# Performance work log

Hardware: AMD Instinct MI355X
Metric: run time of the kernel (lower is better)

The kernel has to match this reference:

```python
import jax, jax.numpy as jnp
import numpy as np

N = 40000          # nodes
E = 400000         # edges (avg degree 10)
MUL0, MUL1 = 64, 32   # 64x0e + 32x1o
RAD, HID = 8, 64      # fc_neurons = [8, 64]
WNUM = 192            # tp.weight_numel = 64+64+32+32
NUM_NEIGHBORS = 10.0
INV3 = 1.0 / np.sqrt(3.0)   # wigner coeff for 1o x 1o -> 0e


def _lin(s, v, Ws, Wv, attr):
    """FullyConnectedTensorProduct(x, 1x0e attr) == per-irrep linear, fan-in normalized."""
    out_s = (s @ Ws) * attr * (1.0 / np.sqrt(Ws.shape[0]))
    out_v = jnp.einsum('nud,uv->nvd', v, Wv) * attr[..., None] * (1.0 / np.sqrt(Wv.shape[0]))
    return out_s, out_v


def setup_inputs() -> dict:
    key = jax.random.key(0)
    ks = jax.random.split(key, 16)
    return {
        'node_input':   jax.random.normal(ks[0], (N, MUL0 + 3 * MUL1), jnp.float32),
        'node_attr':    jnp.ones((N, 1), jnp.float32),
        'edge_attr':    jax.random.normal(ks[1], (E, 4), jnp.float32),   # 1x0e + 1x1o
        'edge_scalars': jax.random.uniform(ks[2], (E, RAD), jnp.float32),
        'W_sc_s': jax.random.normal(ks[3], (MUL0, MUL0), jnp.float32),
        'W_sc_v': jax.random.normal(ks[4], (MUL1, MUL1), jnp.float32),
        'W1_s':   jax.random.normal(ks[5], (MUL0, MUL0), jnp.float32),
        'W1_v':   jax.random.normal(ks[6], (MUL1, MUL1), jnp.float32),
        'W2_s':   jax.random.normal(ks[7], (MUL0 + MUL1, MUL0), jnp.float32),
        'W2_v':   jax.random.normal(ks[8], (MUL0 + MUL1, MUL1), jnp.float32),
        'W3':     jax.random.normal(ks[9], (MUL0 + MUL1, 1), jnp.float32),
        'fcW1':   jax.random.normal(ks[10], (RAD, HID), jnp.float32),
        'fcW2':   jax.random.normal(ks[11], (HID, WNUM), jnp.float32),
        'edge_src': jax.random.randint(ks[12], (E,), 0, N, jnp.int32),
        'edge_dst': jax.random.randint(ks[13], (E,), 0, N, jnp.int32),
    }


def reference(node_input, node_attr, edge_attr, edge_scalars,
              W_sc_s, W_sc_v, W1_s, W1_v, W2_s, W2_v, W3, fcW1, fcW2,
              edge_src, edge_dst):
    n = node_input.shape[0]
    s_in = node_input[:, :MUL0]                       # (N, 64)   0e
    v_in = node_input[:, MUL0:].reshape(n, MUL1, 3)   # (N, 32,3) 1o

    # self connection + first linear (FCTP with 1x0e attr)
    sc_s, sc_v = _lin(s_in, v_in, W_sc_s, W_sc_v, node_attr)
    f_s,  f_v  = _lin(s_in, v_in, W1_s,  W1_v,  node_attr)

    # radial MLP -> per-edge tensor-product weights (silu, fan-in normalized)
    h = jax.nn.silu(edge_scalars @ fcW1 * (1.0 / np.sqrt(RAD)))
    w = h @ fcW2 * (1.0 / np.sqrt(HID))               # (E, 192)
    wA, wB, wC, wD = w[:, :64], w[:, 64:128], w[:, 128:160], w[:, 160:192]

    # gather source node features
    xs = f_s[edge_src]                                # (E, 64)
    xv = f_v[edge_src]                                # (E, 32, 3)
    y0 = edge_attr[:, :1]                             # (E, 1)  0e
    y1 = edge_attr[:, 1:4]                            # (E, 3)  1o

    # 'uvu' tensor-product paths -> irreps_mid = 64x0e + 32x0e + 64x1o + 32x1o
    outA = wA * xs * y0                                            # 0e x 0e -> 0e
    outD = wD * jnp.einsum('eud,ed->eu', xv, y1) * INV3            # 1o x 1o -> 0e
    outB = wB[:, :, None] * xs[:, :, None] * y1[:, None, :]       # 0e x 1o -> 1o
    outC = wC[:, :, None] * xv * y0[:, :, None]                    # 1o x 0e -> 1o
    edge_feat = jnp.concatenate(
        [outA, outD, outB.reshape(-1, MUL0 * 3), outC.reshape(-1, MUL1 * 3)], axis=1)  # (E, 384)

    # scatter_add into destination nodes, normalized by sqrt(num_neighbors)
    agg = jax.ops.segment_sum(edge_feat, edge_dst, num_segments=n)
    agg = agg * (1.0 / np.sqrt(NUM_NEIGHBORS))

    ms = agg[:, :MUL0 + MUL1]                               # (N, 96)   0e
    mv = agg[:, MUL0 + MUL1:].reshape(n, MUL0 + MUL1, 3)    # (N, 96,3) 1o

    # lin2: mid -> output ; lin3: mid -> 0e (scalars only)
    c_s, c_v = _lin(ms, mv, W2_s, W2_v, node_attr)
    conv = jnp.concatenate([c_s, c_v.reshape(n, -1)], axis=1)
    sc   = jnp.concatenate([sc_s, sc_v.reshape(n, -1)], axis=1)
    angle = 0.1 * (ms @ W3) * node_attr * (1.0 / np.sqrt(MUL0 + MUL1))  # (N, 1)

    # sc.output_mask is all-ones here (every output irrep has a path)
    cos, sin = jnp.cos(angle), jnp.sin(angle)
    return cos * sc + sin * conv
```

## Files before the change

### kernel.cpp

```cpp
#include <hip/hip_runtime.h>
#include <math.h>

#define MUL0 64
#define MUL1 32
#define RADF 8
#define HIDF 64
#define WNUM 192
#define NODE_F 160
#define AGG_F  384
#define SWS 200

#define INV_SQRT64 0.125f
#define INV_SQRT32 0.17677669529663687f
#define INV_SQRT8  0.35355339059327373f
#define INV_SQRT96 0.10206207261596575f
#define INV_SQRT10 0.31622776601683794f
#define INV_SQRT3  0.5773502691896258f

typedef __attribute__((ext_vector_type(8))) short bf16x8;
typedef __attribute__((ext_vector_type(4))) float f32x4;

__device__ __forceinline__ float bf2f(unsigned short u) {
    return __uint_as_float((unsigned)u << 16);
}
__device__ __forceinline__ unsigned short f2bfu(float x) {
    unsigned ua = __float_as_uint(x);
    return (unsigned short)((ua + 0x7FFF + ((ua >> 16) & 1)) >> 16);
}
__device__ __forceinline__ unsigned bf16pack(float a, float b) {
    unsigned ua = __float_as_uint(a);
    unsigned ub = __float_as_uint(b);
    ua = (ua + 0x7FFF + ((ua >> 16) & 1)) >> 16;
    ub = (ub + 0x7FFF + ((ub >> 16) & 1)) >> 16;
    return ua | (ub << 16);
}
__device__ __forceinline__ int rdlane(int v, int i) {
    return __builtin_amdgcn_readlane(v, i);
}
__device__ __forceinline__ float rdlanef(float v, int i) {
    return __int_as_float(__builtin_amdgcn_readlane(__float_as_int(v), i));
}
__device__ __forceinline__ bf16x8 cvt8(float4 a, float4 b) {
    union { unsigned q[4]; bf16x8 v; } r;
    r.q[0] = bf16pack(a.x, a.y);
    r.q[1] = bf16pack(a.z, a.w);
    r.q[2] = bf16pack(b.x, b.y);
    r.q[3] = bf16pack(b.z, b.w);
    return r.v;
}

__global__ __launch_bounds__(256) void k_node_lin(
    const float* __restrict__ node_input,
    const float* __restrict__ node_attr,
    const float* __restrict__ W1_s,
    const float* __restrict__ W1_v,
    unsigned short* __restrict__ f, int N)
{
    __shared__ unsigned short s_w1s[8 * 64 * 8];
    __shared__ unsigned short s_w1v[4 * 32 * 8];
    int tid = threadIdx.x;

    for (int task = tid; task < 8 * 64; task += 256) {
        int col = task & 63, koct = task >> 6;
        const float* wp = W1_s + (size_t)(koct * 8) * MUL0 + col;
        unsigned pk0 = bf16pack(wp[0 * MUL0] * INV_SQRT64, wp[1 * MUL0] * INV_SQRT64);
        unsigned pk1 = bf16pack(wp[2 * MUL0] * INV_SQRT64, wp[3 * MUL0] * INV_SQRT64);
        unsigned pk2 = bf16pack(wp[4 * MUL0] * INV_SQRT64, wp[5 * MUL0] * INV_SQRT64);
        unsigned pk3 = bf16pack(wp[6 * MUL0] * INV_SQRT64, wp[7 * MUL0] * INV_SQRT64);
        *(uint4*)&s_w1s[task * 8] = make_uint4(pk0, pk1, pk2, pk3);
    }
    for (int task = tid; task < 4 * 32; task += 256) {
        int col = task & 31, koct = task >> 5;
        const float* wp = W1_v + (size_t)(koct * 8) * MUL1 + col;
        unsigned pk0 = bf16pack(wp[0 * MUL1] * INV_SQRT32, wp[1 * MUL1] * INV_SQRT32);
        unsigned pk1 = bf16pack(wp[2 * MUL1] * INV_SQRT32, wp[3 * MUL1] * INV_SQRT32);
        unsigned pk2 = bf16pack(wp[4 * MUL1] * INV_SQRT32, wp[5 * MUL1] * INV_SQRT32);
        unsigned pk3 = bf16pack(wp[6 * MUL1] * INV_SQRT32, wp[7 * MUL1] * INV_SQRT32);
        *(uint4*)&s_w1v[task * 8] = make_uint4(pk0, pk1, pk2, pk3);
    }
    __syncthreads();

    int lane = tid & 63;
    int wv = tid >> 6;
    int l15 = lane & 15, lh = lane >> 4;
    int ntiles = (N + 15) >> 4;

    for (int tile = blockIdx.x * 4 + wv; tile < ntiles; tile += gridDim.x * 4) {
        int n0 = tile << 4;
        int m = min(16, N - n0);
        int nrow = n0 + min(l15, m - 1);
        const float* inn = node_input + (size_t)nrow * NODE_F;

        float attr[4];
        #pragma unroll
        for (int r = 0; r < 4; ++r)
            attr[r] = node_attr[n0 + min(lh * 4 + r, m - 1)];

        bf16x8 inS[2];
        #pragma unroll
        for (int kk = 0; kk < 2; ++kk) {
            const float* p0 = inn + kk * 32 + lh * 8;
            inS[kk] = cvt8(*(const float4*)p0, *(const float4*)(p0 + 4));
        }
        #pragma unroll
        for (int cb = 0; cb < 4; ++cb) {
            f32x4 a = {0.f, 0.f, 0.f, 0.f};
            #pragma unroll
            for (int kk = 0; kk < 2; ++kk) {
                bf16x8 b = *(const bf16x8*)&s_w1s[(((kk * 4 + lh) * 64) + cb * 16 + l15) * 8];
                a = __builtin_amdgcn_mfma_f32_16x16x32_bf16(inS[kk], b, a, 0, 0, 0);
            }
            #pragma unroll
            for (int r = 0; r < 4; ++r) {
                int node = lh * 4 + r;
                if (node < m)
                    f[(size_t)(n0 + node) * NODE_F + cb * 16 + l15] = f2bfu(a[r] * attr[r]);
            }
        }

        #pragma unroll
        for (int d = 0; d < 3; ++d) {
            float t[8];
            #pragma unroll
            for (int j = 0; j < 8; ++j)
                t[j] = inn[64 + (lh * 8 + j) * 3 + d];
            bf16x8 inV = cvt8(make_float4(t[0], t[1], t[2], t[3]),
                              make_float4(t[4], t[5], t[6], t[7]));
            #pragma unroll
            for (int cb = 0; cb < 2; ++cb) {
                bf16x8 b = *(const bf16x8*)&s_w1v[((lh * 32) + cb * 16 + l15) * 8];
                f32x4 a = {0.f, 0.f, 0.f, 0.f};
                a = __builtin_amdgcn_mfma_f32_16x16x32_bf16(inV, b, a, 0, 0, 0);
                #pragma unroll
                for (int r = 0; r < 4; ++r) {
                    int node = lh * 4 + r;
                    if (node < m)
                        f[(size_t)(n0 + node) * NODE_F + 64 + d * 32 + cb * 16 + l15] =
                            f2bfu(a[r] * attr[r]);
                }
            }
        }
    }
}

__global__ void k_count(const int* __restrict__ edge_dst, int* deg, int E)
{
    int e = blockIdx.x * blockDim.x + threadIdx.x;
    if (e < E) atomicAdd(&deg[edge_dst[e]], 1);
}

__global__ __launch_bounds__(1024) void k_scan_a(const int* __restrict__ deg,
                                                 int* __restrict__ off,
                                                 int* __restrict__ bsum, int N)
{
    __shared__ int swsum[16];
    __shared__ int swoff[16];
    __shared__ int stot;
    int lane = threadIdx.x & 63, wid = threadIdx.x >> 6;
    int ng4 = (N + 3) >> 2;
    int g = blockIdx.x * 1024 + threadIdx.x;
    int4 v = make_int4(0, 0, 0, 0);
    if (g < ng4) v = ((const int4*)deg)[g];
    int s = v.x + v.y + v.z + v.w;
    int val = s;
    #pragma unroll
    for (int sh = 1; sh < 64; sh <<= 1) {
        int t = __shfl_up(val, sh);
        if (lane >= sh) val += t;
    }
    if (lane == 63) swsum[wid] = val;
    __syncthreads();
    if (threadIdx.x < 16) {
        int x = swsum[threadIdx.x];
        int xv = x;
        #pragma unroll
        for (int sh = 1; sh < 16; sh <<= 1) {
            int t = __shfl_up(xv, sh);
            if ((int)threadIdx.x >= sh) xv += t;
        }
        swoff[threadIdx.x] = xv - x;
        if (threadIdx.x == 15) stot = xv;
    }
    __syncthreads();
    if (g < ng4) {
        int b0 = swoff[wid] + (val - s);
        int4 o;
        o.x = b0; o.y = b0 + v.x; o.z = o.y + v.y; o.w = o.z + v.z;
        ((int4*)off)[g] = o;
    }
    if (threadIdx.x == 0) bsum[blockIdx.x] = stot;
}

__global__ __launch_bounds__(1024) void k_scan_b(int* __restrict__ off,
                                                 int* __restrict__ cur,
                                                 const int* __restrict__ bsum,
                                                 int N, int nb)
{
    __shared__ int sbase;
    if (threadIdx.x == 0) {
        int s = 0;
        for (int j = 0; j < (int)blockIdx.x; ++j) s += bsum[j];
        sbase = s;
    }
    __syncthreads();
    int base = sbase;
    int ng4 = (N + 3) >> 2;
    int g = blockIdx.x * 1024 + threadIdx.x;
    if (g < ng4) {
        int4 o = ((int4*)off)[g];
        o.x += base; o.y += base; o.z += base; o.w += base;
        ((int4*)off)[g] = o;
        ((int4*)cur)[g] = o;
    }
}

__global__ void k_scatter(const int* __restrict__ edge_dst,
                          int* cur, int* __restrict__ csr, int E)
{
    int e = blockIdx.x * blockDim.x + threadIdx.x;
    if (e < E) {
        int d = edge_dst[e];
        int pos = atomicAdd(&cur[d], 1);
        csr[pos] = e;
    }
}

#define FLUSH_AGG(node, AT)                                          \
    do {                                                             \
        float* an = agg + (size_t)(node) * AGG_F;                    \
        if (AT) {                                                    \
            atomicAdd(&an[lane], accA);                              \
            atomicAdd(&an[96  + lane], accB0);                       \
            atomicAdd(&an[192 + lane], accB1);                       \
            atomicAdd(&an[288 + lane], accB2);                       \
            if (lane < 32) {                                         \
                atomicAdd(&an[160 + u], accX0);                      \
                atomicAdd(&an[256 + u], accX1);                      \
                atomicAdd(&an[352 + u], accX2);                      \
            } else {                                                 \
                atomicAdd(&an[64 + u], accX0);                       \
            }                                                        \
        } else {                                                     \
            an[lane] = accA;                                         \
            an[96  + lane] = accB0;                                  \
            an[192 + lane] = accB1;                                  \
            an[288 + lane] = accB2;                                  \
            if (lane < 32) {                                         \
                an[160 + u] = accX0;                                 \
                an[256 + u] = accX1;                                 \
                an[352 + u] = accX2;                                 \
            } else {                                                 \
                an[64 + u] = accX0;                                  \
            }                                                        \
        }                                                            \
    } while (0)

__global__ __launch_bounds__(512, 2) void k_edge_fused(
    const unsigned short* __restrict__ f,
    const float* __restrict__ edge_scalars,
    const float* __restrict__ edge_attr,
    const float* __restrict__ fcW1,
    const float* __restrict__ fcW2,
    const int* __restrict__ edge_src,
    const int* __restrict__ edge_dst,
    const int* __restrict__ csr,
    const int* __restrict__ off,
    float* agg, int E)
{
    __shared__ unsigned short s_w2t[8 * 192 * 8];
    __shared__ unsigned short s_w[8][16 * SWS];
    __shared__ float s_fcW1[512];
    __shared__ float4 s_ea8[8][16];

    int tid  = threadIdx.x;
    int lane = tid & 63;
    int wv   = tid >> 6;
    int l15  = lane & 15, lh = lane >> 4;
    int u    = lane & 31;

    for (int task = tid; task < 1536; task += 512) {
        int col = task % 192, oct = task / 192;
        const float* wp = fcW2 + (size_t)(oct * 8) * WNUM + col;
        unsigned pk0 = bf16pack(wp[0 * WNUM], wp[1 * WNUM]);
        unsigned pk1 = bf16pack(wp[2 * WNUM], wp[3 * WNUM]);
        unsigned pk2 = bf16pack(wp[4 * WNUM], wp[5 * WNUM]);
        unsigned pk3 = bf16pack(wp[6 * WNUM], wp[7 * WNUM]);
        *(uint4*)&s_w2t[oct * 1536 + col * 8] = make_uint4(pk0, pk1, pk2, pk3);
    }
    for (int i = tid; i < 512; i += 512)
        s_fcW1[i] = fcW1[i];
    __syncthreads();

    unsigned short* sw = s_w[wv];
    float4* sea = s_ea8[wv];
    int nwt = (E + 15) >> 4;
    int stride8 = gridDim.x * 8;

    int wt = blockIdx.x * 8 + wv;
    if (wt >= nwt) return;

    int P = wt << 4;
    int m = min(16, E - P);
    int e0 = csr[P + min(l15, m - 1)];
    int src = edge_src[e0];
    int dst = edge_dst[e0];
    float4 ea = *(const float4*)(edge_attr + (size_t)e0 * 4);
    float4 es0, es1;
    {
        const float4* esp = (const float4*)(edge_scalars + (size_t)e0 * RADF);
        es0 = esp[0]; es1 = esp[1];
    }

    while (true) {
        if (lh == 0) sea[l15] = ea;

        int firstd = rdlane(dst, 0);
        int lastd  = rdlane(dst, m - 1);
        int off_first = off[firstd];
        int off_last  = off[lastd + 1];

        int wt_n = wt + stride8;
        bool hn = wt_n < nwt;
        int P_n = hn ? (wt_n << 4) : 0;
        int m_n = hn ? min(16, E - P_n) : 1;

        int e_n = csr[hn ? (P_n + min(l15, m_n - 1)) : 0];

        float xs[16], xv0[16], xv1[16], xv2[16];
        #pragma unroll
        for (int i = 0; i < 16; ++i) {
            int si = rdlane(src, i);
            const unsigned short* fb = f + (size_t)si * NODE_F;
            xs[i]  = bf2f(fb[lane]);
            xv0[i] = bf2f(fb[64 + u]);
            xv1[i] = bf2f(fb[96 + u]);
            xv2[i] = bf2f(fb[128 + u]);
        }

        float es[8] = {es0.x, es0.y, es0.z, es0.w, es1.x, es1.y, es1.z, es1.w};
        union { unsigned q[4]; bf16x8 v; } A0, A1;
        #pragma unroll
        for (int jp = 0; jp < 4; ++jp) {
            int k0 = lh * 8 + 2 * jp;
            float aL0 = 0.f, aL1 = 0.f, aH0 = 0.f, aH1 = 0.f;
            #pragma unroll
            for (int r = 0; r < 8; ++r) {
                float2 wl = *(const float2*)&s_fcW1[r * 64 + k0];
                float2 wh = *(const float2*)&s_fcW1[r * 64 + 32 + k0];
                aL0 = fmaf(es[r], wl.x, aL0);
                aL1 = fmaf(es[r], wl.y, aL1);
                aH0 = fmaf(es[r], wh.x, aH0);
                aH1 = fmaf(es[r], wh.y, aH1);
            }
            aL0 *= INV_SQRT8; aL1 *= INV_SQRT8; aH0 *= INV_SQRT8; aH1 *= INV_SQRT8;
            aL0 = aL0 / (1.f + __expf(-aL0));
            aL1 = aL1 / (1.f + __expf(-aL1));
            aH0 = aH0 / (1.f + __expf(-aH0));
            aH1 = aH1 / (1.f + __expf(-aH1));
            A0.q[jp] = bf16pack(aL0, aL1);
            A1.q[jp] = bf16pack(aH0, aH1);
        }

        int src_n = edge_src[e_n];
        int dst_n = edge_dst[e_n];
        float4 ea_n = *(const float4*)(edge_attr + (size_t)e_n * 4);
        float4 es0_n, es1_n;
        {
            const float4* espn = (const float4*)(edge_scalars + (size_t)e_n * RADF);
            es0_n = espn[0]; es1_n = espn[1];
        }

        #pragma unroll
        for (int cb = 0; cb < 12; ++cb) {
            bf16x8 b0 = *(const bf16x8*)&s_w2t[ lh      * 1536 + (cb * 16 + l15) * 8];
            bf16x8 b1 = *(const bf16x8*)&s_w2t[(4 + lh) * 1536 + (cb * 16 + l15) * 8];
            f32x4 acc = {0.f, 0.f, 0.f, 0.f};
            acc = __builtin_amdgcn_mfma_f32_16x16x32_bf16(A0.v, b0, acc, 0, 0, 0);
            acc = __builtin_amdgcn_mfma_f32_16x16x32_bf16(A1.v, b1, acc, 0, 0, 0);
            #pragma unroll
            for (int r = 0; r < 4; ++r)
                sw[(lh * 4 + r) * SWS + cb * 16 + l15] = f2bfu(acc[r] * INV_SQRT64);
        }

        float accA = 0.f, accB0 = 0.f, accB1 = 0.f, accB2 = 0.f;
        float accX0 = 0.f, accX1 = 0.f, accX2 = 0.f;
        int curd = rdlane(dst, 0);
        #pragma unroll
        for (int i = 0; i < 16; ++i) {
            if (i < m) {
                int di = rdlane(dst, i);
                if (di != curd) {
                    bool at = (curd == firstd) && (off_first < P);
                    FLUSH_AGG(curd, at);
                    accA = accB0 = accB1 = accB2 = 0.f;
                    accX0 = accX1 = accX2 = 0.f;
                    curd = di;
                }
                float4 eav = sea[i];
                float W0 = bf2f(sw[i * SWS + lane]);
                float W1 = bf2f(sw[i * SWS + 64 + lane]);
                float W2 = bf2f(sw[i * SWS + 128 + lane]);
                accA = fmaf(W0 * xs[i], eav.x, accA);
                float bx = W1 * xs[i];
                accB0 = fmaf(bx, eav.y, accB0);
                accB1 = fmaf(bx, eav.z, accB1);
                accB2 = fmaf(bx, eav.w, accB2);
                if (lane < 32) {
                    float cc = W2 * eav.x;
                    accX0 = fmaf(cc, xv0[i], accX0);
                    accX1 = fmaf(cc, xv1[i], accX1);
                    accX2 = fmaf(cc, xv2[i], accX2);
                } else {
                    float dv = xv0[i] * eav.y + xv1[i] * eav.z + xv2[i] * eav.w;
                    accX0 = fmaf(W2 * INV_SQRT3, dv, accX0);
                }
            }
        }
        {
            bool at_fin = ((curd == firstd) && (off_first < P)) || (off_last > P + m);
            FLUSH_AGG(curd, at_fin);
        }

        if (!hn) break;
        wt = wt_n; P = P_n; m = m_n;
        src = src_n; dst = dst_n; ea = ea_n; es0 = es0_n; es1 = es1_n;
    }
}

__global__ __launch_bounds__(256) void k_out(
    const float* __restrict__ node_input,
    const float* __restrict__ node_attr,
    const float* __restrict__ agg,
    const float* __restrict__ W_sc_s,
    const float* __restrict__ W_sc_v,
    const float* __restrict__ W2_s,
    const float* __restrict__ W2_v,
    const float* __restrict__ W3,
    float* __restrict__ out, int N)
{
    __shared__ unsigned short s_w2s[12 * 64 * 8];
    __shared__ unsigned short s_wss[ 8 * 64 * 8];
    __shared__ unsigned short s_w2v[12 * 32 * 8];
    __shared__ unsigned short s_wsv[ 4 * 32 * 8];
    __shared__ unsigned short s_w3 [12 * 16 * 8];

    const float pre = INV_SQRT10 * INV_SQRT96;
    int tid = threadIdx.x;

    for (int task = tid; task < 12 * 64; task += 256) {
        int col = task & 63, koct = task >> 6;
        const float* wp = W2_s + (size_t)(koct * 8) * MUL0 + col;
        unsigned pk0 = bf16pack(wp[0 * MUL0] * pre, wp[1 * MUL0] * pre);
        unsigned pk1 = bf16pack(wp[2 * MUL0] * pre, wp[3 * MUL0] * pre);
        unsigned pk2 = bf16pack(wp[4 * MUL0] * pre, wp[5 * MUL0] * pre);
        unsigned pk3 = bf16pack(wp[6 * MUL0] * pre, wp[7 * MUL0] * pre);
        *(uint4*)&s_w2s[task * 8] = make_uint4(pk0, pk1, pk2, pk3);
    }
    for (int task = tid; task < 8 * 64; task += 256) {
        int col = task & 63, koct = task >> 6;
        const float* wp = W_sc_s + (size_t)(koct * 8) * MUL0 + col;
        unsigned pk0 = bf16pack(wp[0 * MUL0] * INV_SQRT64, wp[1 * MUL0] * INV_SQRT64);
        unsigned pk1 = bf16pack(wp[2 * MUL0] * INV_SQRT64, wp[3 * MUL0] * INV_SQRT64);
        unsigned pk2 = bf16pack(wp[4 * MUL0] * INV_SQRT64, wp[5 * MUL0] * INV_SQRT64);
        unsigned pk3 = bf16pack(wp[6 * MUL0] * INV_SQRT64, wp[7 * MUL0] * INV_SQRT64);
        *(uint4*)&s_wss[task * 8] = make_uint4(pk0, pk1, pk2, pk3);
    }
    for (int task = tid; task < 12 * 32; task += 256) {
        int col = task & 31, koct = task >> 5;
        const float* wp = W2_v + (size_t)(koct * 8) * MUL1 + col;
        unsigned pk0 = bf16pack(wp[0 * MUL1] * pre, wp[1 * MUL1] * pre);
        unsigned pk1 = bf16pack(wp[2 * MUL1] * pre, wp[3 * MUL1] * pre);
        unsigned pk2 = bf16pack(wp[4 * MUL1] * pre, wp[5 * MUL1] * pre);
        unsigned pk3 = bf16pack(wp[6 * MUL1] * pre, wp[7 * MUL1] * pre);
        *(uint4*)&s_w2v[task * 8] = make_uint4(pk0, pk1, pk2, pk3);
    }
    for (int task = tid; task < 4 * 32; task += 256) {
        int col = task & 31, koct = task >> 5;
        const float* wp = W_sc_v + (size_t)(koct * 8) * MUL1 + col;
        unsigned pk0 = bf16pack(wp[0 * MUL1] * INV_SQRT32, wp[1 * MUL1] * INV_SQRT32);
        unsigned pk1 = bf16pack(wp[2 * MUL1] * INV_SQRT32, wp[3 * MUL1] * INV_SQRT32);
        unsigned pk2 = bf16pack(wp[4 * MUL1] * INV_SQRT32, wp[5 * MUL1] * INV_SQRT32);
        unsigned pk3 = bf16pack(wp[6 * MUL1] * INV_SQRT32, wp[7 * MUL1] * INV_SQRT32);
        *(uint4*)&s_wsv[task * 8] = make_uint4(pk0, pk1, pk2, pk3);
    }
    for (int task = tid; task < 12 * 16; task += 256) {
        int col = task & 15, koct = task >> 4;
        const float sc3 = 0.1f * pre;
        unsigned pk0 = 0, pk1 = 0, pk2 = 0, pk3 = 0;
        if (col == 0) {
            const float* wp = W3 + koct * 8;
            pk0 = bf16pack(wp[0] * sc3, wp[1] * sc3);
            pk1 = bf16pack(wp[2] * sc3, wp[3] * sc3);
            pk2 = bf16pack(wp[4] * sc3, wp[5] * sc3);
            pk3 = bf16pack(wp[6] * sc3, wp[7] * sc3);
        }
        *(uint4*)&s_w3[task * 8] = make_uint4(pk0, pk1, pk2, pk3);
    }
    __syncthreads();

    int lane = tid & 63;
    int wv = tid >> 6;
    int l15 = lane & 15, lh = lane >> 4;
    int ntiles = (N + 15) >> 4;

    for (int tile = blockIdx.x * 4 + wv; tile < ntiles; tile += gridDim.x * 4) {
        int n0 = tile << 4;
        int m = min(16, N - n0);
        int nrow = n0 + min(l15, m - 1);
        const float* agn = agg + (size_t)nrow * AGG_F;
        const float* inn = node_input + (size_t)nrow * NODE_F;

        bf16x8 aggA[3], inS[2];
        #pragma unroll
        for (int kk = 0; kk < 3; ++kk) {
            const float* p0 = agn + kk * 32 + lh * 8;
            aggA[kk] = cvt8(*(const float4*)p0, *(const float4*)(p0 + 4));
        }
        #pragma unroll
        for (int kk = 0; kk < 2; ++kk) {
            const float* p0 = inn + kk * 32 + lh * 8;
            inS[kk] = cvt8(*(const float4*)p0, *(const float4*)(p0 + 4));
        }

        f32x4 convS[4], scS[4], angD = {0.f, 0.f, 0.f, 0.f};
        #pragma unroll
        for (int cb = 0; cb < 4; ++cb) {
            f32x4 a = {0.f, 0.f, 0.f, 0.f};
            #pragma unroll
            for (int kk = 0; kk < 3; ++kk) {
                bf16x8 b = *(const bf16x8*)&s_w2s[(((kk * 4 + lh) * 64) + cb * 16 + l15) * 8];
                a = __builtin_amdgcn_mfma_f32_16x16x32_bf16(aggA[kk], b, a, 0, 0, 0);
            }
            convS[cb] = a;
            f32x4 s = {0.f, 0.f, 0.f, 0.f};
            #pragma unroll
            for (int kk = 0; kk < 2; ++kk) {
                bf16x8 b = *(const bf16x8*)&s_wss[(((kk * 4 + lh) * 64) + cb * 16 + l15) * 8];
                s = __builtin_amdgcn_mfma_f32_16x16x32_bf16(inS[kk], b, s, 0, 0, 0);
            }
            scS[cb] = s;
        }
        #pragma unroll
        for (int kk = 0; kk < 3; ++kk) {
            bf16x8 b = *(const bf16x8*)&s_w3[(((kk * 4 + lh) * 16) + l15) * 8];
            angD = __builtin_amdgcn_mfma_f32_16x16x32_bf16(aggA[kk], b, angD, 0, 0, 0);
        }

        float attr[4], cs[4], sn[4];
        #pragma unroll
        for (int r = 0; r < 4; ++r) {
            attr[r] = node_attr[n0 + min(lh * 4 + r, m - 1)];
            float ang = __shfl(angD[r], lane & 48) * attr[r];
            cs[r] = cosf(ang);
            sn[r] = sinf(ang);
        }

        #pragma unroll
        for (int cb = 0; cb < 4; ++cb)
            #pragma unroll
            for (int r = 0; r < 4; ++r) {
                int node = lh * 4 + r;
                if (node < m)
                    out[(size_t)(n0 + node) * NODE_F + cb * 16 + l15] =
                        attr[r] * (cs[r] * scS[cb][r] + sn[r] * convS[cb][r]);
            }

        #pragma unroll
        for (int d = 0; d < 3; ++d) {
            bf16x8 aggV[3], inV;
            #pragma unroll
            for (int kk = 0; kk < 3; ++kk) {
                const float* p0 = agn + 96 + d * 96 + kk * 32 + lh * 8;
                aggV[kk] = cvt8(*(const float4*)p0, *(const float4*)(p0 + 4));
            }
            {
                float t[8];
                #pragma unroll
                for (int j = 0; j < 8; ++j)
                    t[j] = inn[64 + (lh * 8 + j) * 3 + d];
                inV = cvt8(make_float4(t[0], t[1], t[2], t[3]),
                           make_float4(t[4], t[5], t[6], t[7]));
            }
            #pragma unroll
            for (int cb = 0; cb < 2; ++cb) {
                f32x4 a = {0.f, 0.f, 0.f, 0.f};
                #pragma unroll
                for (int kk = 0; kk < 3; ++kk) {
                    bf16x8 b = *(const bf16x8*)&s_w2v[(((kk * 4 + lh) * 32) + cb * 16 + l15) * 8];
                    a = __builtin_amdgcn_mfma_f32_16x16x32_bf16(aggV[kk], b, a, 0, 0, 0);
                }
                f32x4 s = {0.f, 0.f, 0.f, 0.f};
                {
                    bf16x8 b = *(const bf16x8*)&s_wsv[((lh * 32) + cb * 16 + l15) * 8];
                    s = __builtin_amdgcn_mfma_f32_16x16x32_bf16(inV, b, s, 0, 0, 0);
                }
                #pragma unroll
                for (int r = 0; r < 4; ++r) {
                    int node = lh * 4 + r;
                    if (node < m)
                        out[(size_t)(n0 + node) * NODE_F + 64 + (cb * 16 + l15) * 3 + d] =
                            attr[r] * (cs[r] * s[r] + sn[r] * a[r]);
                }
            }
        }
    }
}

extern "C" void kernel_launch(void* const* d_in, const int* in_sizes, int n_in,
                              void* d_out, int out_size, void* d_ws, size_t ws_size,
                              hipStream_t stream)
{
    const float* node_input   = (const float*)d_in[0];
    const float* node_attr    = (const float*)d_in[1];
    const float* edge_attr    = (const float*)d_in[2];
    const float* edge_scalars = (const float*)d_in[3];
    const float* W_sc_s       = (const float*)d_in[4];
    const float* W_sc_v       = (const float*)d_in[5];
    const float* W1_s         = (const float*)d_in[6];
    const float* W1_v         = (const float*)d_in[7];
    const float* W2_s         = (const float*)d_in[8];
    const float* W2_v         = (const float*)d_in[9];
    const float* W3           = (const float*)d_in[10];
    const float* fcW1         = (const float*)d_in[11];
    const float* fcW2         = (const float*)d_in[12];
    const int*   edge_src     = (const int*)d_in[13];
    const int*   edge_dst     = (const int*)d_in[14];
    float* out = (float*)d_out;

    const int N = in_sizes[1];
    const int E = in_sizes[13];
    const int Np = (N + 3) & ~3;

    char* p = (char*)d_ws;
    float* agg = (float*)p;            p += (size_t)N * AGG_F * sizeof(float);
    unsigned short* fbf = (unsigned short*)p;  p += (size_t)N * NODE_F * sizeof(unsigned short);
    int*   deg = (int*)p;              p += (size_t)Np * sizeof(int);
    int*   cur = (int*)p;              p += (size_t)Np * sizeof(int);
    int*   off = (int*)p;              p += (size_t)(Np + 4) * sizeof(int);
    int*   csr = (int*)p;              p += (size_t)E * sizeof(int);
    int*   bsum = (int*)p;             p += 64 * sizeof(int);

    hipMemsetAsync(deg, 0, (size_t)Np * sizeof(int), stream);
    hipMemsetAsync(agg, 0, (size_t)N * AGG_F * sizeof(float), stream);

    int eb = (E + 255) / 256;
    k_count<<<eb, 256, 0, stream>>>(edge_dst, deg, E);

    int ng4 = (N + 3) >> 2;
    int nb = (ng4 + 1023) / 1024;
    k_scan_a<<<nb, 1024, 0, stream>>>(deg, off, bsum, N);
    k_scan_b<<<nb, 1024, 0, stream>>>(off, cur, bsum, N, nb);
    k_scatter<<<eb, 256, 0, stream>>>(edge_dst, cur, csr, E);

    int ntiles = (N + 15) / 16;
    int gridL = (ntiles + 3) / 4;
    k_node_lin<<<gridL, 256, 0, stream>>>(node_input, node_attr, W1_s, W1_v, fbf, N);

    int nwt = (E + 15) / 16;
    int gridF = (nwt + 7) / 8;
    if (gridF > 1024) gridF = 1024;
    k_edge_fused<<<gridF, 512, 0, stream>>>(fbf, edge_scalars, edge_attr, fcW1, fcW2,
                                            edge_src, edge_dst, csr, off, agg, E);

    int gridO = (ntiles + 3) / 4;
    if (gridO > 640) gridO = 640;
    k_out<<<gridO, 256, 0, stream>>>(node_input, node_attr, agg,
                                     W_sc_s, W_sc_v, W2_s, W2_v, W3, out, N);
}
```

Baseline: 220.4 us.

## Replace boundary atomics with per-tile bf16 overflow buffer and drop agg memset

When a destination node's edges span several 16-edge tiles, each later tile now writes its partial sum as bf16 into a per-tile overflow slot instead of using float atomics on agg. The output kernel adds those overflow slots back in, using the CSR offsets to find them. The full memset of agg is removed; the scan kernel zeroes only rows of nodes with no edges, and the bf16 node features are staged in the output buffer. This avoids atomic traffic and a large memset, at the cost of extra reads in the output kernel, bf16 rounding of the partial sums, and relying on the output buffer as scratch space.

```diff
diff --git a/kernel.cpp b/kernel.cpp
--- a/kernel.cpp
+++ b/kernel.cpp
@@ -37,9 +37,6 @@
 __device__ __forceinline__ int rdlane(int v, int i) {
     return __builtin_amdgcn_readlane(v, i);
 }
-__device__ __forceinline__ float rdlanef(float v, int i) {
-    return __int_as_float(__builtin_amdgcn_readlane(__float_as_int(v), i));
-}
 __device__ __forceinline__ bf16x8 cvt8(float4 a, float4 b) {
     union { unsigned q[4]; bf16x8 v; } r;
     r.q[0] = bf16pack(a.x, a.y);
@@ -47,6 +44,22 @@
     r.q[2] = bf16pack(b.x, b.y);
     r.q[3] = bf16pack(b.z, b.w);
     return r.v;
+}
+__device__ __forceinline__ bf16x8 load8ovf(const float* agn,
+                                           const unsigned short* ovf16,
+                                           int tA, int tB, int base)
+{
+    float4 a = *(const float4*)(agn + base);
+    float4 b = *(const float4*)(agn + base + 4);
+    float v[8] = {a.x, a.y, a.z, a.w, b.x, b.y, b.z, b.w};
+    for (int t = tA; t <= tB; ++t) {
+        const unsigned short* ov = ovf16 + (size_t)t * AGG_F + base;
+        #pragma unroll
+        for (int j = 0; j < 8; ++j)
+            v[j] += bf2f(ov[j]);
+    }
+    return cvt8(make_float4(v[0], v[1], v[2], v[3]),
+                make_float4(v[4], v[5], v[6], v[7]));
 }
 
 __global__ __launch_bounds__(256) void k_node_lin(
@@ -194,6 +207,8 @@
 __global__ __launch_bounds__(1024) void k_scan_b(int* __restrict__ off,
                                                  int* __restrict__ cur,
                                                  const int* __restrict__ bsum,
+                                                 float* __restrict__ agg,
+                                                 const int* __restrict__ deg,
                                                  int N, int nb)
 {
     __shared__ int sbase;
@@ -211,6 +226,18 @@
         o.x += base; o.y += base; o.z += base; o.w += base;
         ((int4*)off)[g] = o;
         ((int4*)cur)[g] = o;
+        int4 d = ((const int4*)deg)[g];
+        int n0 = g * 4;
+        #pragma unroll
+        for (int q = 0; q < 4; ++q) {
+            int dq = (q == 0) ? d.x : (q == 1) ? d.y : (q == 2) ? d.z : d.w;
+            int nq = n0 + q;
+            if (dq == 0 && nq < N) {
+                float4* row = (float4*)(agg + (size_t)nq * AGG_F);
+                float4 z = make_float4(0.f, 0.f, 0.f, 0.f);
+                for (int j = 0; j < AGG_F / 4; ++j) row[j] = z;
+            }
+        }
     }
 }
 
@@ -225,22 +252,23 @@
     }
 }
 
-#define FLUSH_AGG(node, AT)                                          \
+#define FLUSH_AGG(node, OVF)                                         \
     do {                                                             \
-        float* an = agg + (size_t)(node) * AGG_F;                    \
-        if (AT) {                                                    \
-            atomicAdd(&an[lane], accA);                              \
-            atomicAdd(&an[96  + lane], accB0);                       \
-            atomicAdd(&an[192 + lane], accB1);                       \
-            atomicAdd(&an[288 + lane], accB2);                       \
+        if (OVF) {                                                   \
+            unsigned short* ov = ovf16 + (size_t)wt * AGG_F;         \
+            ov[lane] = f2bfu(accA);                                  \
+            ov[96  + lane] = f2bfu(accB0);                           \
+            ov[192 + lane] = f2bfu(accB1);                           \
+            ov[288 + lane] = f2bfu(accB2);                           \
             if (lane < 32) {                                         \
-                atomicAdd(&an[160 + u], accX0);                      \
-                atomicAdd(&an[256 + u], accX1);                      \
-                atomicAdd(&an[352 + u], accX2);                      \
+                ov[160 + u] = f2bfu(accX0);                          \
+                ov[256 + u] = f2bfu(accX1);                          \
+                ov[352 + u] = f2bfu(accX2);                          \
             } else {                                                 \
-                atomicAdd(&an[64 + u], accX0);                       \
+                ov[64 + u] = f2bfu(accX0);                           \
             }                                                        \
         } else {                                                     \
+            float* an = agg + (size_t)(node) * AGG_F;                \
             an[lane] = accA;                                         \
             an[96  + lane] = accB0;                                  \
             an[192 + lane] = accB1;                                  \
@@ -265,7 +293,8 @@
     const int* __restrict__ edge_dst,
     const int* __restrict__ csr,
     const int* __restrict__ off,
-    float* agg, int E)
+    float* __restrict__ agg,
+    unsigned short* __restrict__ ovf16, int E)
 {
     __shared__ unsigned short s_w2t[8 * 192 * 8];
     __shared__ unsigned short s_w[8][16 * SWS];
@@ -315,9 +344,7 @@
         if (lh == 0) sea[l15] = ea;
 
         int firstd = rdlane(dst, 0);
-        int lastd  = rdlane(dst, m - 1);
         int off_first = off[firstd];
-        int off_last  = off[lastd + 1];
 
         int wt_n = wt + stride8;
         bool hn = wt_n < nwt;
@@ -390,8 +417,8 @@
             if (i < m) {
                 int di = rdlane(dst, i);
                 if (di != curd) {
-                    bool at = (curd == firstd) && (off_first < P);
-                    FLUSH_AGG(curd, at);
+                    bool ov = (curd == firstd) && (off_first < P);
+                    FLUSH_AGG(curd, ov);
                     accA = accB0 = accB1 = accB2 = 0.f;
                     accX0 = accX1 = accX2 = 0.f;
                     curd = di;
@@ -417,8 +444,8 @@
             }
         }
         {
-            bool at_fin = ((curd == firstd) && (off_first < P)) || (off_last > P + m);
-            FLUSH_AGG(curd, at_fin);
+            bool ov_fin = (curd == firstd) && (off_first < P);
+            FLUSH_AGG(curd, ov_fin);
         }
 
         if (!hn) break;
@@ -431,6 +458,8 @@
     const float* __restrict__ node_input,
     const float* __restrict__ node_attr,
     const float* __restrict__ agg,
+    const unsigned short* __restrict__ ovf16,
+    const int* __restrict__ off,
     const float* __restrict__ W_sc_s,
     const float* __restrict__ W_sc_v,
     const float* __restrict__ W2_s,
@@ -510,12 +539,14 @@
         const float* agn = agg + (size_t)nrow * AGG_F;
         const float* inn = node_input + (size_t)nrow * NODE_F;
 
+        int o0 = off[nrow], o1 = off[nrow + 1];
+        int tA = (o0 >> 4) + 1;
+        int tB = (o1 > o0) ? ((o1 - 1) >> 4) : (tA - 1);
+
         bf16x8 aggA[3], inS[2];
         #pragma unroll
-        for (int kk = 0; kk < 3; ++kk) {
-            const float* p0 = agn + kk * 32 + lh * 8;
-            aggA[kk] = cvt8(*(const float4*)p0, *(const float4*)(p0 + 4));
-        }
+        for (int kk = 0; kk < 3; ++kk)
+            aggA[kk] = load8ovf(agn, ovf16, tA, tB, kk * 32 + lh * 8);
         #pragma unroll
         for (int kk = 0; kk < 2; ++kk) {
             const float* p0 = inn + kk * 32 + lh * 8;
@@ -569,10 +600,8 @@
         for (int d = 0; d < 3; ++d) {
             bf16x8 aggV[3], inV;
             #pragma unroll
-            for (int kk = 0; kk < 3; ++kk) {
-                const float* p0 = agn + 96 + d * 96 + kk * 32 + lh * 8;
-                aggV[kk] = cvt8(*(const float4*)p0, *(const float4*)(p0 + 4));
-            }
+            for (int kk = 0; kk < 3; ++kk)
+                aggV[kk] = load8ovf(agn, ovf16, tA, tB, 96 + d * 96 + kk * 32 + lh * 8);
             {
                 float t[8];
                 #pragma unroll
@@ -630,18 +659,21 @@
     const int N = in_sizes[1];
     const int E = in_sizes[13];
     const int Np = (N + 3) & ~3;
+    const int nwt = (E + 15) / 16;
 
     char* p = (char*)d_ws;
     float* agg = (float*)p;            p += (size_t)N * AGG_F * sizeof(float);
-    unsigned short* fbf = (unsigned short*)p;  p += (size_t)N * NODE_F * sizeof(unsigned short);
     int*   deg = (int*)p;              p += (size_t)Np * sizeof(int);
     int*   cur = (int*)p;              p += (size_t)Np * sizeof(int);
     int*   off = (int*)p;              p += (size_t)(Np + 4) * sizeof(int);
     int*   csr = (int*)p;              p += (size_t)E * sizeof(int);
     int*   bsum = (int*)p;             p += 64 * sizeof(int);
+    p = (char*)(((size_t)p + 15) & ~(size_t)15);
+    unsigned short* ovf16 = (unsigned short*)p;
+
+    unsigned short* fbf = (unsigned short*)d_out;
 
     hipMemsetAsync(deg, 0, (size_t)Np * sizeof(int), stream);
-    hipMemsetAsync(agg, 0, (size_t)N * AGG_F * sizeof(float), stream);
 
     int eb = (E + 255) / 256;
     k_count<<<eb, 256, 0, stream>>>(edge_dst, deg, E);
@@ -649,21 +681,20 @@
     int ng4 = (N + 3) >> 2;
     int nb = (ng4 + 1023) / 1024;
     k_scan_a<<<nb, 1024, 0, stream>>>(deg, off, bsum, N);
-    k_scan_b<<<nb, 1024, 0, stream>>>(off, cur, bsum, N, nb);
+    k_scan_b<<<nb, 1024, 0, stream>>>(off, cur, bsum, agg, deg, N, nb);
     k_scatter<<<eb, 256, 0, stream>>>(edge_dst, cur, csr, E);
 
     int ntiles = (N + 15) / 16;
     int gridL = (ntiles + 3) / 4;
     k_node_lin<<<gridL, 256, 0, stream>>>(node_input, node_attr, W1_s, W1_v, fbf, N);
 
-    int nwt = (E + 15) / 16;
     int gridF = (nwt + 7) / 8;
     if (gridF > 1024) gridF = 1024;
     k_edge_fused<<<gridF, 512, 0, stream>>>(fbf, edge_scalars, edge_attr, fcW1, fcW2,
-                                            edge_src, edge_dst, csr, off, agg, E);
+                                            edge_src, edge_dst, csr, off, agg, ovf16, E);
 
     int gridO = (ntiles + 3) / 4;
     if (gridO > 640) gridO = 640;
-    k_out<<<gridO, 256, 0, stream>>>(node_input, node_attr, agg,
+    k_out<<<gridO, 256, 0, stream>>>(node_input, node_attr, agg, ovf16, off,
                                      W_sc_s, W_sc_v, W2_s, W2_v, W3, out, N);
 }
```

After: 210.3 us. 1.05x faster.
